# Performance work log

Measured on AMD Instinct MI355X. Metric: run time of the kernel, lower is better.

## Reference

```python
import jax, jax.numpy as jnp
import numpy as np

B, S, D = 4, 4096, 256


def setup_inputs() -> dict:
    key = jax.random.key(0)
    ks = jax.random.split(key, 8)
    inv = 1.0 / np.sqrt(D)
    return {
        "input_tensor": jax.random.normal(ks[0], (B, S, D), dtype=jnp.float32),
        "attention_mask": jax.random.randint(ks[1], (B, S, S), 0, 2) == 1,
        "Wq": jax.random.uniform(ks[2], (D, D), jnp.float32, -inv, inv),
        "bq": jax.random.uniform(ks[3], (D,), jnp.float32, -inv, inv),
        "Wk": jax.random.uniform(ks[4], (D, D), jnp.float32, -inv, inv),
        "bk": jax.random.uniform(ks[5], (D,), jnp.float32, -inv, inv),
        "Wv": jax.random.uniform(ks[6], (D, D), jnp.float32, -inv, inv),
        "bv": jax.random.uniform(ks[7], (D,), jnp.float32, -inv, inv),
    }


def reference(input_tensor, attention_mask, Wq, bq, Wk, bk, Wv, bv):
    # Linear projections: y = x @ W.T + b  (nn.Linear convention, W is [out,in])
    query = jnp.einsum("bsd,ed->bse", input_tensor, Wq) + bq
    key = jnp.einsum("bsd,ed->bse", input_tensor, Wk) + bk
    value = jnp.einsum("bsd,ed->bse", input_tensor, Wv) + bv
    # Faithful quirk: original scales by sqrt(query.size(1)) == sqrt(seq_len)
    scale = jnp.asarray(query.shape[1], query.dtype) ** 0.5
    scores = jnp.einsum("bqd,bkd->bqk", query, key) / scale  # [B,S,S]
    scores = jnp.where(attention_mask, jnp.asarray(-1e9, scores.dtype), scores)
    attn = jax.nn.softmax(scores, axis=-1)
    # dropout with p=0.0 is identity (eval-mode reference)
    context = jnp.einsum("bqk,bkd->bqd", attn, value)
    return context
```

## Files before the change

kernel.cpp:

```cpp
#include <hip/hip_runtime.h>
#include <hip/hip_bf16.h>
#include <stdint.h>

#define BB 4
#define SS 4096
#define DD 256

typedef __attribute__((ext_vector_type(4))) float f32x4;
typedef __attribute__((ext_vector_type(8))) short s16x8;

__device__ __forceinline__ ushort f2bf(float f) {
  __hip_bfloat16 h = __float2bfloat16(f);
  return __builtin_bit_cast(ushort, h);
}

__global__ void convert_kernel(const float* __restrict__ X,
                               const float* __restrict__ Wq,
                               const float* __restrict__ Wk,
                               const float* __restrict__ Wv,
                               const float* __restrict__ bq,
                               const float* __restrict__ bk,
                               const float* __restrict__ bv,
                               ushort* __restrict__ Xb,
                               ushort* __restrict__ Wb,
                               float* __restrict__ bias) {
  int tid = blockIdx.x * blockDim.x + threadIdx.x;
  int stride = gridDim.x * blockDim.x;
  const int NX4 = (BB * SS * DD) / 4;
  for (int i = tid; i < NX4; i += stride) {
    float4 v = ((const float4*)X)[i];
    ushort4 o = { f2bf(v.x), f2bf(v.y), f2bf(v.z), f2bf(v.w) };
    ((ushort4*)Xb)[i] = o;
  }
  const int NW4 = (DD * DD) / 4;
  for (int i = tid; i < NW4; i += stride) {
    float4 a = ((const float4*)Wq)[i];
    float4 b = ((const float4*)Wk)[i];
    float4 c = ((const float4*)Wv)[i];
    ushort4 oa = { f2bf(a.x), f2bf(a.y), f2bf(a.z), f2bf(a.w) };
    ushort4 ob = { f2bf(b.x), f2bf(b.y), f2bf(b.z), f2bf(b.w) };
    ushort4 oc = { f2bf(c.x), f2bf(c.y), f2bf(c.z), f2bf(c.w) };
    ((ushort4*)Wb)[i]           = oa;
    ((ushort4*)Wb)[NW4 + i]     = ob;
    ((ushort4*)Wb)[2 * NW4 + i] = oc;
  }
  if (tid < DD) {
    bias[tid]          = bq[tid];
    bias[DD + tid]     = bk[tid];
    bias[2 * DD + tid] = bv[tid];
  }
}

#define LROW 40

__global__ __launch_bounds__(256) void proj_gemm(const ushort* __restrict__ Xb,
                                                 const ushort* __restrict__ Wb,
                                                 const float* __restrict__ bias,
                                                 ushort* __restrict__ Qb,
                                                 ushort* __restrict__ Kb,
                                                 ushort* __restrict__ Vt) {
  __shared__ ushort Al[128 * LROW];
  __shared__ ushort Bl[128 * LROW];
  const int m0 = blockIdx.x * 128;
  const int n0 = blockIdx.y * 128;
  const int t = threadIdx.x;
  const int lane = t & 63;
  const int w = t >> 6;
  const int wr = w & 1, wc = w >> 1;
  const int col = lane & 15;
  const int quad = lane >> 4;

  f32x4 acc[4][4];
#pragma unroll
  for (int i = 0; i < 4; i++)
#pragma unroll
    for (int j = 0; j < 4; j++) acc[i][j] = f32x4{0.f, 0.f, 0.f, 0.f};

  const int ci0 = t, ci1 = 256 + t;
  const int r0 = ci0 >> 2, c0 = ci0 & 3;
  const int r1 = ci1 >> 2, c1 = ci1 & 3;

  s16x8 pa0 = *(const s16x8*)(Xb + (m0 + r0) * DD + c0 * 8);
  s16x8 pa1 = *(const s16x8*)(Xb + (m0 + r1) * DD + c1 * 8);
  s16x8 pb0 = *(const s16x8*)(Wb + (n0 + r0) * DD + c0 * 8);
  s16x8 pb1 = *(const s16x8*)(Wb + (n0 + r1) * DD + c1 * 8);

  for (int kk = 0; kk < DD; kk += 32) {
    __syncthreads();
    *(s16x8*)&Al[r0 * LROW + c0 * 8] = pa0;
    *(s16x8*)&Al[r1 * LROW + c1 * 8] = pa1;
    *(s16x8*)&Bl[r0 * LROW + c0 * 8] = pb0;
    *(s16x8*)&Bl[r1 * LROW + c1 * 8] = pb1;
    __syncthreads();
    const int kn = kk + 32;
    if (kn < DD) {
      pa0 = *(const s16x8*)(Xb + (m0 + r0) * DD + kn + c0 * 8);
      pa1 = *(const s16x8*)(Xb + (m0 + r1) * DD + kn + c1 * 8);
      pb0 = *(const s16x8*)(Wb + (n0 + r0) * DD + kn + c0 * 8);
      pb1 = *(const s16x8*)(Wb + (n0 + r1) * DD + kn + c1 * 8);
    }
    s16x8 af[4], bfr[4];
#pragma unroll
    for (int mi = 0; mi < 4; mi++)
      af[mi] = *(const s16x8*)&Al[(wr * 64 + mi * 16 + col) * LROW + quad * 8];
#pragma unroll
    for (int ni = 0; ni < 4; ni++)
      bfr[ni] = *(const s16x8*)&Bl[(wc * 64 + ni * 16 + col) * LROW + quad * 8];
#pragma unroll
    for (int mi = 0; mi < 4; mi++)
#pragma unroll
      for (int ni = 0; ni < 4; ni++)
        acc[mi][ni] = __builtin_amdgcn_mfma_f32_16x16x32_bf16(af[mi], bfr[ni], acc[mi][ni], 0, 0, 0);
  }

  const int region = n0 >> 8;
#pragma unroll
  for (int mi = 0; mi < 4; mi++) {
    const int gm = m0 + wr * 64 + mi * 16 + quad * 4;
#pragma unroll
    for (int ni = 0; ni < 4; ni++) {
      const int gn = n0 + wc * 64 + ni * 16 + col;
      const float bb = bias[gn];
      f32x4 v = acc[mi][ni];
      if (region == 0) {
#pragma unroll
        for (int rg = 0; rg < 4; rg++)
          Qb[(gm + rg) * DD + gn] = f2bf((v[rg] + bb) * 0.015625f);
      } else if (region == 1) {
        const int d = gn - 256;
#pragma unroll
        for (int rg = 0; rg < 4; rg++)
          Kb[(gm + rg) * DD + d] = f2bf(v[rg] + bb);
      } else {
        const int d = gn - 512;
        const int b = gm >> 12;
        const int s = gm & (SS - 1);
        ushort4 o = { f2bf(v[0] + bb), f2bf(v[1] + bb), f2bf(v[2] + bb), f2bf(v[3] + bb) };
        *(ushort4*)&Vt[((size_t)(b << 8) + d) * SS + s] = o;
      }
    }
  }
}

#define NKT 32
#define KROW 264
#define VROW 32
#define PROW 32

#define KL_U (NKT * KROW)
#define VL_U (DD * VROW)
#define PL_U (16 * PROW)
#define VOFF (2 * KL_U)
#define POFF (VOFF + 2 * VL_U)
#define SM_U (POFF + 8 * PL_U)

#define XSTRIDE 72

__global__ __launch_bounds__(512) void attn_kernel(const ushort* __restrict__ Qb,
                                                   const ushort* __restrict__ Kb,
                                                   const ushort* __restrict__ Vt,
                                                   const int* __restrict__ mask,
                                                   float* __restrict__ out,
                                                   float* __restrict__ O1,
                                                   float* __restrict__ Ml) {
  __shared__ __align__(16) ushort sm[SM_U];

  const int qt = blockIdx.x;
  const int b = blockIdx.y;
  const int z = blockIdx.z;
  const int t = threadIdx.x;
  const int g = t >> 8;
  const int tg = t & 255;
  const int lane = t & 63;
  const int w = tg >> 6;
  const int w8 = t >> 6;
  const int col = lane & 15;
  const int quad = lane >> 4;

  ushort* Kl = sm + g * KL_U;
  ushort* Vl = sm + VOFF + g * VL_U;
  ushort* Pw = sm + POFF + w8 * PL_U;

  const int q0 = qt * 64;
  const int qrow = q0 + w * 16;

  s16x8 qf[8];
  {
    const ushort* qp = Qb + ((size_t)b * SS + qrow + col) * DD + quad * 8;
#pragma unroll
    for (int dc = 0; dc < 8; dc++) qf[dc] = *(const s16x8*)(qp + dc * 32);
  }

  int kr[4], kc[4], vd[4], vc[4];
#pragma unroll
  for (int i = 0; i < 4; i++) {
    const int ci = i * 256 + tg;
    kr[i] = ci >> 5; kc[i] = ci & 31;
    vd[i] = ci >> 2; vc[i] = ci & 3;
  }

  const ushort* Kg = Kb + (size_t)b * SS * DD;
  const ushort* Vg = Vt + (size_t)b * DD * SS;
  const int* Mg = mask + ((size_t)b * SS + qrow + quad * 4) * SS;

  f32x4 Oc[16];
#pragma unroll
  for (int i = 0; i < 16; i++) Oc[i] = f32x4{0.f, 0.f, 0.f, 0.f};
  float m_i[4] = {-INFINITY, -INFINITY, -INFINITY, -INFINITY};
  float l_i[4] = {0.f, 0.f, 0.f, 0.f};

  const int NT2 = 1024 / NKT;
  const int kb0 = z * 2048 + g * 1024;

  s16x8 pk[4], pv[4];
  int pm[2][4];
#pragma unroll
  for (int i = 0; i < 4; i++) {
    pk[i] = *(const s16x8*)(Kg + (size_t)(kb0 + kr[i]) * DD + kc[i] * 8);
    pv[i] = *(const s16x8*)(Vg + (size_t)vd[i] * SS + kb0 + vc[i] * 8);
  }
#pragma unroll
  for (int jt = 0; jt < 2; jt++)
#pragma unroll
    for (int rg = 0; rg < 4; rg++) pm[jt][rg] = Mg[rg * SS + kb0 + jt * 16 + col];

  for (int tt = 0; tt < NT2; tt++) {
    __syncthreads();
#pragma unroll
    for (int i = 0; i < 4; i++) {
      *(s16x8*)&Kl[kr[i] * KROW + kc[i] * 8] = pk[i];
      *(s16x8*)&Vl[vd[i] * VROW + vc[i] * 8] = pv[i];
    }
    __syncthreads();
    int mcur[2][4];
#pragma unroll
    for (int jt = 0; jt < 2; jt++)
#pragma unroll
      for (int rg = 0; rg < 4; rg++) mcur[jt][rg] = pm[jt][rg];
    if (tt + 1 < NT2) {
      const int k0n = kb0 + (tt + 1) * NKT;
#pragma unroll
      for (int i = 0; i < 4; i++) {
        pk[i] = *(const s16x8*)(Kg + ((size_t)k0n + kr[i]) * DD + kc[i] * 8);
        pv[i] = *(const s16x8*)(Vg + (size_t)vd[i] * SS + k0n + vc[i] * 8);
      }
#pragma unroll
      for (int jt = 0; jt < 2; jt++)
#pragma unroll
        for (int rg = 0; rg < 4; rg++) pm[jt][rg] = Mg[rg * SS + k0n + jt * 16 + col];
    }

    f32x4 st[2];
    __builtin_amdgcn_s_setprio(1);
#pragma unroll
    for (int jt = 0; jt < 2; jt++) {
      f32x4 s = f32x4{0.f, 0.f, 0.f, 0.f};
#pragma unroll
      for (int dc = 0; dc < 8; dc++) {
        s16x8 kb = *(const s16x8*)&Kl[(jt * 16 + col) * KROW + dc * 32 + quad * 8];
        s = __builtin_amdgcn_mfma_f32_16x16x32_bf16(qf[dc], kb, s, 0, 0, 0);
      }
      st[jt] = s;
    }
    __builtin_amdgcn_s_setprio(0);
#pragma unroll
    for (int jt = 0; jt < 2; jt++)
#pragma unroll
      for (int rg = 0; rg < 4; rg++)
        if (mcur[jt][rg]) st[jt][rg] = -1e9f;

    float al[4];
#pragma unroll
    for (int rg = 0; rg < 4; rg++) {
      float v = fmaxf(st[0][rg], st[1][rg]);
      v = fmaxf(v, __shfl_xor(v, 1));
      v = fmaxf(v, __shfl_xor(v, 2));
      v = fmaxf(v, __shfl_xor(v, 4));
      v = fmaxf(v, __shfl_xor(v, 8));
      const float mn = fmaxf(m_i[rg], v);
      al[rg] = __expf(m_i[rg] - mn);
      m_i[rg] = mn;
    }
#pragma unroll
    for (int rg = 0; rg < 4; rg++) {
      const float p0 = __expf(st[0][rg] - m_i[rg]);
      const float p1 = __expf(st[1][rg] - m_i[rg]);
      st[0][rg] = p0; st[1][rg] = p1;
      float s2 = p0 + p1;
      s2 += __shfl_xor(s2, 1);
      s2 += __shfl_xor(s2, 2);
      s2 += __shfl_xor(s2, 4);
      s2 += __shfl_xor(s2, 8);
      l_i[rg] = l_i[rg] * al[rg] + s2;
    }
#pragma unroll
    for (int dt = 0; dt < 16; dt++)
#pragma unroll
      for (int rg = 0; rg < 4; rg++) Oc[dt][rg] *= al[rg];

#pragma unroll
    for (int jt = 0; jt < 2; jt++)
#pragma unroll
      for (int rg = 0; rg < 4; rg++)
        Pw[(quad * 4 + rg) * PROW + jt * 16 + col] = f2bf(st[jt][rg]);
    s16x8 pa = *(const s16x8*)&Pw[col * PROW + quad * 8];

    __builtin_amdgcn_s_setprio(1);
#pragma unroll
    for (int dt = 0; dt < 16; dt++) {
      s16x8 vb = *(const s16x8*)&Vl[(dt * 16 + col) * VROW + quad * 8];
      Oc[dt] = __builtin_amdgcn_mfma_f32_16x16x32_bf16(pa, vb, Oc[dt], 0, 0, 0);
    }
    __builtin_amdgcn_s_setprio(0);
  }

  __syncthreads();
  float* ex = (float*)sm;
  float* slot = ex + (size_t)(w * 64 + lane) * XSTRIDE;
  if (g == 1) {
#pragma unroll
    for (int rg = 0; rg < 4; rg++) { slot[rg] = m_i[rg]; slot[4 + rg] = l_i[rg]; }
#pragma unroll
    for (int dt = 0; dt < 16; dt++) *(f32x4*)&slot[8 + dt * 4] = Oc[dt];
  }
  __syncthreads();
  if (g == 0) {
    float a0[4], a1[4];
#pragma unroll
    for (int rg = 0; rg < 4; rg++) {
      const float m1 = slot[rg];
      const float l1 = slot[4 + rg];
      const float mm = fmaxf(m_i[rg], m1);
      a0[rg] = __expf(m_i[rg] - mm);
      a1[rg] = __expf(m1 - mm);
      m_i[rg] = mm;
      l_i[rg] = l_i[rg] * a0[rg] + l1 * a1[rg];
    }
    float* op = (z ? O1 : out) + ((size_t)b * SS + qrow + quad * 4) * DD;
#pragma unroll
    for (int dt = 0; dt < 16; dt++) {
      const f32x4 o1 = *(const f32x4*)&slot[8 + dt * 4];
#pragma unroll
      for (int rg = 0; rg < 4; rg++)
        op[rg * DD + dt * 16 + col] = Oc[dt][rg] * a0[rg] + o1[rg] * a1[rg];
    }
    if (col == 0) {
      float2* pml = (float2*)Ml + (size_t)z * BB * SS + (size_t)b * SS + qrow + quad * 4;
#pragma unroll
      for (int rg = 0; rg < 4; rg++) pml[rg] = make_float2(m_i[rg], l_i[rg]);
    }
  }
}

__global__ __launch_bounds__(256) void merge_kernel(const float* __restrict__ Ml,
                                                    const float* __restrict__ O1,
                                                    float* __restrict__ out) {
  const int row = blockIdx.x * 4 + (threadIdx.x >> 6);
  const int lane = threadIdx.x & 63;
  const float2 ml0 = ((const float2*)Ml)[row];
  const float2 ml1 = ((const float2*)Ml)[BB * SS + row];
  const float mm = fmaxf(ml0.x, ml1.x);
  const float a0 = __expf(ml0.x - mm);
  const float a1 = __expf(ml1.x - mm);
  const float inv = 1.0f / (ml0.y * a0 + ml1.y * a1);
  f32x4* po = (f32x4*)out + (size_t)row * 64 + lane;
  const f32x4 o0 = *po;
  const f32x4 o1 = ((const f32x4*)O1)[(size_t)row * 64 + lane];
  f32x4 r;
#pragma unroll
  for (int j = 0; j < 4; j++) r[j] = (o0[j] * a0 + o1[j] * a1) * inv;
  *po = r;
}

extern "C" void kernel_launch(void* const* d_in, const int* in_sizes, int n_in,
                              void* d_out, int out_size, void* d_ws, size_t ws_size,
                              hipStream_t stream) {
  const float* X  = (const float*)d_in[0];
  const int* mask = (const int*)d_in[1];
  const float* Wq = (const float*)d_in[2];
  const float* bq = (const float*)d_in[3];
  const float* Wk = (const float*)d_in[4];
  const float* bk = (const float*)d_in[5];
  const float* Wv = (const float*)d_in[6];
  const float* bv = (const float*)d_in[7];
  float* out = (float*)d_out;

  ushort* base = (ushort*)d_ws;
  ushort* Xb = base;
  ushort* Wb = Xb + (size_t)BB * SS * DD;
  ushort* Qb = Wb + (size_t)3 * DD * DD;
  ushort* Kb = Qb + (size_t)BB * SS * DD;
  ushort* Vt = Kb + (size_t)BB * SS * DD;
  float* bias = (float*)(Vt + (size_t)BB * SS * DD);
  float* O1 = bias + 768;
  float* Ml = O1 + (size_t)BB * SS * DD;

  convert_kernel<<<1024, 256, 0, stream>>>(X, Wq, Wk, Wv, bq, bk, bv, Xb, Wb, bias);
  proj_gemm<<<dim3(128, 6), 256, 0, stream>>>(Xb, Wb, bias, Qb, Kb, Vt);
  attn_kernel<<<dim3(64, 4, 2), 512, 0, stream>>>(Qb, Kb, Vt, mask, out, O1, Ml);
  merge_kernel<<<(BB * SS) / 4, 256, 0, stream>>>(Ml, O1, out);
}
```

Measured before the change: 540.1 us.

## Alias K and V LDS tiles and split the final cross-group merge

K and V tiles now share one LDS region per group: K is staged, scores are computed, then after an extra barrier V overwrites the same buffer before the PV MFMAs. This shrinks shared memory per block, apparently to allow more resident blocks per CU, and the epilogue exchange is split into two rounds so it fits in the smaller allocation. The cost is two extra __syncthreads per key tile and V loads that are now serialized behind the QK phase, which reduces overlap.

```diff
diff --git a/kernel.cpp b/kernel.cpp
--- a/kernel.cpp
+++ b/kernel.cpp
@@ -147,11 +147,9 @@
 #define VROW 32
 #define PROW 32
 
-#define KL_U (NKT * KROW)
-#define VL_U (DD * VROW)
+#define KVREG_U 8448
 #define PL_U (16 * PROW)
-#define VOFF (2 * KL_U)
-#define POFF (VOFF + 2 * VL_U)
+#define POFF (2 * KVREG_U)
 #define SM_U (POFF + 8 * PL_U)
 
 #define XSTRIDE 72
@@ -177,8 +175,8 @@
   const int col = lane & 15;
   const int quad = lane >> 4;
 
-  ushort* Kl = sm + g * KL_U;
-  ushort* Vl = sm + VOFF + g * VL_U;
+  ushort* Kl = sm + g * KVREG_U;
+  ushort* Vl = sm + g * KVREG_U;
   ushort* Pw = sm + POFF + w8 * PL_U;
 
   const int q0 = qt * 64;
@@ -227,23 +225,19 @@
   for (int tt = 0; tt < NT2; tt++) {
     __syncthreads();
 #pragma unroll
-    for (int i = 0; i < 4; i++) {
+    for (int i = 0; i < 4; i++)
       *(s16x8*)&Kl[kr[i] * KROW + kc[i] * 8] = pk[i];
-      *(s16x8*)&Vl[vd[i] * VROW + vc[i] * 8] = pv[i];
-    }
     __syncthreads();
     int mcur[2][4];
 #pragma unroll
     for (int jt = 0; jt < 2; jt++)
 #pragma unroll
       for (int rg = 0; rg < 4; rg++) mcur[jt][rg] = pm[jt][rg];
+    const int k0n = kb0 + (tt + 1) * NKT;
     if (tt + 1 < NT2) {
-      const int k0n = kb0 + (tt + 1) * NKT;
-#pragma unroll
-      for (int i = 0; i < 4; i++) {
+#pragma unroll
+      for (int i = 0; i < 4; i++)
         pk[i] = *(const s16x8*)(Kg + ((size_t)k0n + kr[i]) * DD + kc[i] * 8);
-        pv[i] = *(const s16x8*)(Vg + (size_t)vd[i] * SS + k0n + vc[i] * 8);
-      }
 #pragma unroll
       for (int jt = 0; jt < 2; jt++)
 #pragma unroll
@@ -293,10 +287,6 @@
       s2 += __shfl_xor(s2, 8);
       l_i[rg] = l_i[rg] * al[rg] + s2;
     }
-#pragma unroll
-    for (int dt = 0; dt < 16; dt++)
-#pragma unroll
-      for (int rg = 0; rg < 4; rg++) Oc[dt][rg] *= al[rg];
 
 #pragma unroll
     for (int jt = 0; jt < 2; jt++)
@@ -305,6 +295,22 @@
         Pw[(quad * 4 + rg) * PROW + jt * 16 + col] = f2bf(st[jt][rg]);
     s16x8 pa = *(const s16x8*)&Pw[col * PROW + quad * 8];
 
+#pragma unroll
+    for (int dt = 0; dt < 16; dt++)
+#pragma unroll
+      for (int rg = 0; rg < 4; rg++) Oc[dt][rg] *= al[rg];
+
+    __syncthreads();
+#pragma unroll
+    for (int i = 0; i < 4; i++)
+      *(s16x8*)&Vl[vd[i] * VROW + vc[i] * 8] = pv[i];
+    if (tt + 1 < NT2) {
+#pragma unroll
+      for (int i = 0; i < 4; i++)
+        pv[i] = *(const s16x8*)(Vg + (size_t)vd[i] * SS + k0n + vc[i] * 8);
+    }
+    __syncthreads();
+
     __builtin_amdgcn_s_setprio(1);
 #pragma unroll
     for (int dt = 0; dt < 16; dt++) {
@@ -314,35 +320,47 @@
     __builtin_amdgcn_s_setprio(0);
   }
 
-  __syncthreads();
   float* ex = (float*)sm;
-  float* slot = ex + (size_t)(w * 64 + lane) * XSTRIDE;
-  if (g == 1) {
-#pragma unroll
-    for (int rg = 0; rg < 4; rg++) { slot[rg] = m_i[rg]; slot[4 + rg] = l_i[rg]; }
-#pragma unroll
-    for (int dt = 0; dt < 16; dt++) *(f32x4*)&slot[8 + dt * 4] = Oc[dt];
-  }
-  __syncthreads();
+#pragma unroll
+  for (int rr = 0; rr < 2; rr++) {
+    __syncthreads();
+    if (g == 1 && (w >> 1) == rr) {
+      float* slot = ex + (size_t)((w & 1) * 64 + lane) * XSTRIDE;
+#pragma unroll
+      for (int rg = 0; rg < 4; rg++) { slot[rg] = m_i[rg]; slot[4 + rg] = l_i[rg]; }
+#pragma unroll
+      for (int dt = 0; dt < 16; dt++) *(f32x4*)&slot[8 + dt * 4] = Oc[dt];
+    }
+    __syncthreads();
+    if (g == 0 && (w >> 1) == rr) {
+      const float* slot = ex + (size_t)((w & 1) * 64 + lane) * XSTRIDE;
+      float a0[4], a1[4];
+#pragma unroll
+      for (int rg = 0; rg < 4; rg++) {
+        const float m1 = slot[rg];
+        const float l1 = slot[4 + rg];
+        const float mm = fmaxf(m_i[rg], m1);
+        a0[rg] = __expf(m_i[rg] - mm);
+        a1[rg] = __expf(m1 - mm);
+        m_i[rg] = mm;
+        l_i[rg] = l_i[rg] * a0[rg] + l1 * a1[rg];
+      }
+#pragma unroll
+      for (int dt = 0; dt < 16; dt++) {
+        const f32x4 o1 = *(const f32x4*)&slot[8 + dt * 4];
+#pragma unroll
+        for (int rg = 0; rg < 4; rg++)
+          Oc[dt][rg] = Oc[dt][rg] * a0[rg] + o1[rg] * a1[rg];
+      }
+    }
+  }
   if (g == 0) {
-    float a0[4], a1[4];
-#pragma unroll
-    for (int rg = 0; rg < 4; rg++) {
-      const float m1 = slot[rg];
-      const float l1 = slot[4 + rg];
-      const float mm = fmaxf(m_i[rg], m1);
-      a0[rg] = __expf(m_i[rg] - mm);
-      a1[rg] = __expf(m1 - mm);
-      m_i[rg] = mm;
-      l_i[rg] = l_i[rg] * a0[rg] + l1 * a1[rg];
-    }
     float* op = (z ? O1 : out) + ((size_t)b * SS + qrow + quad * 4) * DD;
 #pragma unroll
     for (int dt = 0; dt < 16; dt++) {
-      const f32x4 o1 = *(const f32x4*)&slot[8 + dt * 4];
 #pragma unroll
       for (int rg = 0; rg < 4; rg++)
-        op[rg * DD + dt * 16 + col] = Oc[dt][rg] * a0[rg] + o1[rg] * a1[rg];
+        op[rg * DD + dt * 16 + col] = Oc[dt][rg];
     }
     if (col == 0) {
       float2* pml = (float2*)Ml + (size_t)z * BB * SS + (size_t)b * SS + qrow + quad * 4;
```

After: 513.7 us. 1.05x faster.
